# Performance work log

Hardware: AMD Instinct MI355X
Metric: run time of the kernel (lower is better)

The kernel has to match this reference:

```python
import jax, jax.numpy as jnp
import numpy as np

B, N, C = 16, 1024, 256
SIZE = (512, 640)          # (H, W) image size
STRIDE = 8
H0, W0 = SIZE[0] // STRIDE, SIZE[1] // STRIDE   # 64, 80
P_TOK = H0 * W0                                  # 5120 base tokens
NHEAD, NLVL, NPTS = 8, 4, 4
HD = C // NHEAD
NUM_CLASSES = 7


def setup_inputs() -> dict:
    key = jax.random.key(0)
    ks = jax.random.split(key, 16)
    g = lambda k, shape, s=0.02: jax.random.normal(k, shape, jnp.float32) * s
    return {
        "q_t": jax.random.normal(ks[0], (B, N, C), jnp.float32),
        "h_t": jax.random.normal(ks[1], (B, P_TOK, C), jnp.float32),
        "p_head_t": jax.random.uniform(ks[2], (B, N, 2), jnp.float32)
                    * jnp.array([SIZE[1], SIZE[0]], jnp.float32),  # (x,y) in image coords
        "W_off": g(ks[3], (C, NHEAD * NLVL * NPTS * 2)),
        "b_off": g(ks[4], (NHEAD * NLVL * NPTS * 2,)),
        "W_attn": g(ks[5], (C, NHEAD * NLVL * NPTS)),
        "b_attn": g(ks[6], (NHEAD * NLVL * NPTS,)),
        "W_v": g(ks[7], (C, C)), "b_v": g(ks[8], (C,)),
        "W_o": g(ks[9], (C, C)), "b_o": g(ks[10], (C,)),
        "W_p1": g(ks[11], (2 * C, C)), "b_p1": g(ks[12], (C,)),
        "W_p2": g(ks[13], (C, NUM_CLASSES)), "b_p2": g(ks[14], (NUM_CLASSES,)),
    }


def _bilinear_sample(value_l, loc):
    """value_l: (B,Hl,Wl,nh,hd); loc: (B,N,nh,NPTS,2) in [0,1] normalized (x,y).
    grid_sample semantics: align_corners=False, padding_mode='zeros'.
    Returns (B,nh,N,NPTS,hd)."""
    Bb, Hl, Wl = value_l.shape[0], value_l.shape[1], value_l.shape[2]
    x = loc[..., 0] * Wl - 0.5
    y = loc[..., 1] * Hl - 0.5
    x0 = jnp.floor(x); y0 = jnp.floor(y)
    wx = x - x0; wy = y - y0
    x0i = x0.astype(jnp.int32); y0i = y0.astype(jnp.int32)
    flat = value_l.reshape(Bb, Hl * Wl, NHEAD, HD).transpose(0, 2, 1, 3)  # (B,nh,S,hd)

    def corner(xi, yi):
        valid = ((xi >= 0) & (xi < Wl) & (yi >= 0) & (yi < Hl)).astype(value_l.dtype)
        idx = (jnp.clip(yi, 0, Hl - 1) * Wl + jnp.clip(xi, 0, Wl - 1)).transpose(0, 2, 1, 3)  # (B,nh,N,P)
        g = jnp.take_along_axis(flat, idx.reshape(Bb, NHEAD, -1)[..., None], axis=2)
        g = g.reshape(Bb, NHEAD, idx.shape[2], idx.shape[3], HD)
        return g * valid.transpose(0, 2, 1, 3)[..., None]

    tw = lambda w: w.transpose(0, 2, 1, 3)[..., None]  # (B,nh,N,P,1)
    return (corner(x0i, y0i) * tw((1 - wx) * (1 - wy))
            + corner(x0i + 1, y0i) * tw(wx * (1 - wy))
            + corner(x0i, y0i + 1) * tw((1 - wx) * wy)
            + corner(x0i + 1, y0i + 1) * tw(wx * wy))


def reference(q_t, h_t, p_head_t, W_off, b_off, W_attn, b_attn,
              W_v, b_v, W_o, b_o, W_p1, b_p1, W_p2, b_p2):
    # normalize point predictions to [0,1] (x by W, y by H)
    p_norm = jnp.clip(p_head_t / jnp.array([SIZE[1], SIZE[0]], jnp.float32), 0.0, 1.0)

    # ---- get_deformable_inputs: 4-level pyramid by 2x2 average pooling ----
    cur = h_t.reshape(B, H0, W0, C)
    feats, shapes = [], []
    for l in range(NLVL):
        feats.append(cur)
        shapes.append((cur.shape[1], cur.shape[2]))
        if l < NLVL - 1:
            h, w = cur.shape[1], cur.shape[2]
            cur = cur.reshape(B, h // 2, 2, w // 2, 2, C).mean(axis=(2, 4))
    f_scales = jnp.concatenate([f.reshape(B, -1, C) for f in feats], axis=1)  # (B,S,C)

    # ---- DMSMHA_Block (multi-scale deformable attention) ----
    value = (f_scales @ W_v + b_v).reshape(B, -1, NHEAD, HD)
    offsets = (q_t @ W_off + b_off).reshape(B, N, NHEAD, NLVL, NPTS, 2)
    attn = jax.nn.softmax(
        (q_t @ W_attn + b_attn).reshape(B, N, NHEAD, NLVL * NPTS), axis=-1
    ).reshape(B, N, NHEAD, NLVL, NPTS)

    out = jnp.zeros((B, NHEAD, N, HD), jnp.float32)
    start = 0
    for l, (Hl, Wl) in enumerate(shapes):
        Sl = Hl * Wl
        vl = value[:, start:start + Sl].reshape(B, Hl, Wl, NHEAD, HD)
        start += Sl
        norm = jnp.array([Wl, Hl], jnp.float32)
        loc = p_norm[:, :, None, None, :] + offsets[:, :, :, l] / norm  # (B,N,nh,P,2)
        sampled = _bilinear_sample(vl, loc)                              # (B,nh,N,P,hd)
        w = attn[:, :, :, l].transpose(0, 2, 1, 3)                       # (B,nh,N,P)
        out = out + jnp.einsum('bhnp,bhnpd->bhnd', w, sampled)

    q_local = out.transpose(0, 2, 1, 3).reshape(B, N, C) @ W_o + b_o

    # ---- fuse + MLP head ----
    q_fused = jnp.concatenate([q_t, q_local], axis=-1)
    hid = jax.nn.relu(q_fused @ W_p1 + b_p1)
    logits = hid @ W_p2 + b_p2   # (B,N,num_classes)
    return logits
```

## Files before the change

### kernel.cpp

```cpp
#include <hip/hip_runtime.h>
#include <math.h>


namespace {

constexpr int kB = 16;
constexpr int kN = 1024;
constexpr int kC = 256;
constexpr int kNCLS = 7;
constexpr int kSTOT = 6800;

typedef __attribute__((ext_vector_type(8))) short short8;
typedef __attribute__((ext_vector_type(4))) float f32x4;

__device__ inline ushort f2bf(float f) {
  union { float f; unsigned u; } v; v.f = f;
  unsigned r = (v.u + 0x7fffu + ((v.u >> 16) & 1u)) >> 16;
  return (ushort)r;
}
__device__ inline float bf2f(ushort h) {
  union { unsigned u; float f; } v; v.u = ((unsigned)h) << 16;
  return v.f;
}

__device__ inline void gload16(const ushort* g, ushort* l) {
  __builtin_amdgcn_global_load_lds(
      (const __attribute__((address_space(1))) void*)g,
      (__attribute__((address_space(3))) void*)l, 16, 0, 0);
}

__global__ void cast_f2b_kernel(const float* __restrict__ in, ushort* __restrict__ out, int n4) {
  int i = blockIdx.x * 256 + threadIdx.x;
  if (i >= n4) return;
  float4 v = ((const float4*)in)[i];
  ((ushort4*)out)[i] = make_ushort4(f2bf(v.x), f2bf(v.y), f2bf(v.z), f2bf(v.w));
}

__global__ void cast_pool_kernel(const float* __restrict__ h, ushort* __restrict__ fsc) {
  int i = blockIdx.x * 256 + threadIdx.x;
  if (i >= kB * 32 * 40 * 64) return;
  int cq = i & 63;
  int t = i >> 6;
  int x = t % 40; t /= 40;
  int y = t % 32; int b = t / 32;
  const float* base = h + (((size_t)b * 5120 + (2 * y) * 80 + 2 * x) << 8) + (cq << 2);
  float4 v00 = *(const float4*)(base);
  float4 v01 = *(const float4*)(base + 256);
  float4 v10 = *(const float4*)(base + 80 * 256);
  float4 v11 = *(const float4*)(base + 80 * 256 + 256);
  ushort* f0 = fsc + (((size_t)b * kSTOT + (2 * y) * 80 + 2 * x) << 8) + (cq << 2);
  *(ushort4*)(f0) = make_ushort4(f2bf(v00.x), f2bf(v00.y), f2bf(v00.z), f2bf(v00.w));
  *(ushort4*)(f0 + 256) = make_ushort4(f2bf(v01.x), f2bf(v01.y), f2bf(v01.z), f2bf(v01.w));
  *(ushort4*)(f0 + 80 * 256) = make_ushort4(f2bf(v10.x), f2bf(v10.y), f2bf(v10.z), f2bf(v10.w));
  *(ushort4*)(f0 + 80 * 256 + 256) =
      make_ushort4(f2bf(v11.x), f2bf(v11.y), f2bf(v11.z), f2bf(v11.w));
  float4 pv = make_float4(0.25f * (v00.x + v01.x + v10.x + v11.x),
                          0.25f * (v00.y + v01.y + v10.y + v11.y),
                          0.25f * (v00.z + v01.z + v10.z + v11.z),
                          0.25f * (v00.w + v01.w + v10.w + v11.w));
  ushort* f1 = fsc + (((size_t)b * kSTOT + 5120 + y * 40 + x) << 8) + (cq << 2);
  *(ushort4*)(f1) = make_ushort4(f2bf(pv.x), f2bf(pv.y), f2bf(pv.z), f2bf(pv.w));
}

__global__ void pool_b2b_kernel(const ushort* __restrict__ fin, ushort* __restrict__ fout,
                                int oh, int ow, int so_in, int so_out) {
  int idx = blockIdx.x * 256 + threadIdx.x;
  if (idx >= kB * oh * ow * kC) return;
  int c = idx & 255; int t = idx >> 8;
  int x = t % ow; t /= ow; int y = t % oh; int b = t / oh;
  int iw = ow * 2;
  const ushort* p = fin + (((size_t)b * kSTOT + so_in + y * 2 * iw + x * 2) << 8) + c;
  float s = 0.25f * (bf2f(p[0]) + bf2f(p[256]) + bf2f(p[iw * 256]) + bf2f(p[iw * 256 + 256]));
  fout[(((size_t)b * kSTOT + so_out + y * ow + x) << 8) + c] = f2bf(s);
}

__global__ void wtrans_all_kernel(const float* __restrict__ s0, const float* __restrict__ s1,
                                  const float* __restrict__ s2, const float* __restrict__ s3,
                                  const float* __restrict__ s4,
                                  ushort* __restrict__ d0, ushort* __restrict__ d1,
                                  ushort* __restrict__ d2, ushort* __restrict__ d3,
                                  ushort* __restrict__ d4) {
  __shared__ float t[32][33];
  const float* W; ushort* Wt; int K, N;
  switch (blockIdx.z) {
    case 0: W = s0; Wt = d0; K = 256; N = 256; break;
    case 1: W = s1; Wt = d1; K = 256; N = 256; break;
    case 2: W = s2; Wt = d2; K = 256; N = 128; break;
    case 3: W = s3; Wt = d3; K = 256; N = 256; break;
    default: W = s4; Wt = d4; K = 512; N = 256; break;
  }
  int nx = blockIdx.x << 5, ky = blockIdx.y << 5;
  if (nx >= N || ky >= K) return;
  int lx = threadIdx.x & 31, ly = threadIdx.x >> 5;
#pragma unroll
  for (int i = 0; i < 32; i += 8)
    t[ly + i][lx] = W[(size_t)(ky + ly + i) * N + nx + lx];
  __syncthreads();
#pragma unroll
  for (int i = 0; i < 32; i += 8)
    Wt[(size_t)(nx + ly + i) * K + ky + lx] = f2bf(t[lx][ly + i]);
}

template <int KTOT, bool SPLITK, int OMODE, bool RELU>
__global__ __launch_bounds__(256) void gemm_bf16_kernel(
    const ushort* __restrict__ A, const ushort* __restrict__ A2,
    const ushort* __restrict__ Wt, const float* __restrict__ bias,
    const float* __restrict__ bias2, void* __restrict__ Cout,
    void* __restrict__ Cout2, int ldc) {
  __shared__ ushort Asm[2][128 * 32];
  __shared__ ushort Bsm[2][128 * 32];
  const int tid = threadIdx.x;
  const int w = tid >> 6, l = tid & 63;
  const int bm = blockIdx.y << 7, bn = blockIdx.x << 7;
  const int wm = w >> 1, wn = w & 1;

  const int c0 = w * 2, c1 = w * 2 + 1;
  const int G0 = c0 * 64 + l, G1 = c1 * 64 + l;
  const int r0 = G0 >> 2, g0 = G0 & 3;
  const int r1 = G1 >> 2, g1 = G1 & 3;
  const int sz0 = (g0 ^ ((r0 >> 1) & 3)) << 3;
  const int sz1 = (g1 ^ ((r1 >> 1) & 3)) << 3;
  const int ak = SPLITK ? 256 : KTOT;
  const ushort* sA0 = A + (size_t)(bm + r0) * ak + sz0;
  const ushort* sA1 = A + (size_t)(bm + r1) * ak + sz1;
  const ushort* sA0b = SPLITK ? A2 + (size_t)(bm + r0) * 256 + sz0 : nullptr;
  const ushort* sA1b = SPLITK ? A2 + (size_t)(bm + r1) * 256 + sz1 : nullptr;
  const ushort* sB0 = Wt + (size_t)(bn + r0) * KTOT + sz0;
  const ushort* sB1 = Wt + (size_t)(bn + r1) * KTOT + sz1;

  const int e = l >> 4, rl = l & 15;
  int aoff[4], boff[4];
#pragma unroll
  for (int i = 0; i < 4; ++i) {
    int r = wm * 64 + i * 16 + rl;
    aoff[i] = r * 32 + ((e ^ ((r >> 1) & 3)) << 3);
    int rb = wn * 64 + i * 16 + rl;
    boff[i] = rb * 32 + ((e ^ ((rb >> 1) & 3)) << 3);
  }

  f32x4 acc[4][4];
#pragma unroll
  for (int i = 0; i < 4; ++i)
#pragma unroll
    for (int j = 0; j < 4; ++j) acc[i][j] = (f32x4){0.f, 0.f, 0.f, 0.f};

  auto stage = [&](int buf, int k0) {
    const ushort *a0, *a1;
    if (SPLITK && k0 >= 256) {
      a0 = sA0b + (k0 - 256);
      a1 = sA1b + (k0 - 256);
    } else {
      a0 = sA0 + k0;
      a1 = sA1 + k0;
    }
    gload16(a0, &Asm[buf][c0 * 512]);
    gload16(a1, &Asm[buf][c1 * 512]);
    gload16(sB0 + k0, &Bsm[buf][c0 * 512]);
    gload16(sB1 + k0, &Bsm[buf][c1 * 512]);
  };

  constexpr int nt = KTOT / 32;
  stage(0, 0);
  __syncthreads();
  for (int t = 0; t < nt; ++t) {
    const int cur = t & 1;
    if (t + 1 < nt) stage(cur ^ 1, (t + 1) * 32);
    short8 af[4], bfr[4];
#pragma unroll
    for (int i = 0; i < 4; ++i) af[i] = *(const short8*)&Asm[cur][aoff[i]];
#pragma unroll
    for (int j = 0; j < 4; ++j) bfr[j] = *(const short8*)&Bsm[cur][boff[j]];
#pragma unroll
    for (int i = 0; i < 4; ++i)
#pragma unroll
      for (int j = 0; j < 4; ++j)
        acc[i][j] = __builtin_amdgcn_mfma_f32_16x16x32_bf16(bfr[j], af[i], acc[i][j], 0, 0, 0);
    __syncthreads();
  }

#pragma unroll
  for (int j = 0; j < 4; ++j) {
    int ch = bn + wn * 64 + j * 16 + e * 4;
    float4 b4;
    if (OMODE == 2)
      b4 = (ch < 256) ? *(const float4*)(bias + ch) : *(const float4*)(bias2 + ch - 256);
    else
      b4 = *(const float4*)(bias + ch);
    float bv[4] = {b4.x, b4.y, b4.z, b4.w};
#pragma unroll
    for (int i = 0; i < 4; ++i) {
      int sp = bm + wm * 64 + i * 16 + rl;
      float v[4];
#pragma unroll
      for (int r = 0; r < 4; ++r) {
        v[r] = acc[i][j][r] + bv[r];
        if (RELU) v[r] = fmaxf(v[r], 0.f);
      }
      if (OMODE == 0) {
        *(float4*)&((float*)Cout)[(size_t)sp * ldc + ch] = make_float4(v[0], v[1], v[2], v[3]);
      } else if (OMODE == 1) {
        *(ushort4*)&((ushort*)Cout)[(size_t)sp * ldc + ch] =
            make_ushort4(f2bf(v[0]), f2bf(v[1]), f2bf(v[2]), f2bf(v[3]));
      } else {
        if (ch < 256)
          *(float4*)&((float*)Cout)[(size_t)sp * 256 + ch] = make_float4(v[0], v[1], v[2], v[3]);
        else
          *(float4*)&((float*)Cout2)[(size_t)sp * 128 + (ch - 256)] =
              make_float4(v[0], v[1], v[2], v[3]);
      }
    }
  }
}

__global__ void deform_kernel(
    const ushort* __restrict__ value, const float* __restrict__ off,
    const float* __restrict__ attnl, const float* __restrict__ p_head,
    ushort* __restrict__ samp) {
  int blk = (int)blockIdx.x;
  int sw = (blk & 7) * 256 + (blk >> 3);
  int wvi = (sw << 2) + (threadIdx.x >> 6);
  int l = threadIdx.x & 63;
  int nq = l >> 5;
  int lh = l & 31;
  int h = lh >> 2;
  int pt = wvi * 2 + nq;
  int b = pt >> 10;
  size_t bn = (size_t)pt;

  float ph = (lh < 2) ? p_head[bn * 2 + lh] : 0.f;
  float px = __shfl(ph, (nq << 5) + 0, 64) * (1.0f / 640.0f);
  float py = __shfl(ph, (nq << 5) + 1, 64) * (1.0f / 512.0f);
  px = fminf(fmaxf(px, 0.f), 1.f);
  py = fminf(fmaxf(py, 0.f), 1.f);

  const float4* offp = (const float4*)(off + (bn << 8));
  float4 ofv0 = offp[2 * lh];
  float4 ofv1 = offp[2 * lh + 1];
  float4 atv = ((const float4*)(attnl + (bn << 7)))[lh];

  float m = fmaxf(fmaxf(atv.x, atv.y), fmaxf(atv.z, atv.w));
  m = fmaxf(m, __shfl_xor(m, 1, 64));
  m = fmaxf(m, __shfl_xor(m, 2, 64));
  float e0 = expf(atv.x - m), e1 = expf(atv.y - m);
  float e2 = expf(atv.z - m), e3 = expf(atv.w - m);
  float s = e0 + e1 + e2 + e3;
  s += __shfl_xor(s, 1, 64);
  s += __shfl_xor(s, 2, 64);
  float inv = 1.f / s;
  atv = make_float4(e0 * inv, e1 * inv, e2 * inv, e3 * inv);

  float acc[8];
#pragma unroll
  for (int i = 0; i < 8; ++i) acc[i] = 0.f;
  const ushort* vbb = value + (((size_t)b * kSTOT) << 8) + (lh << 3);

#pragma unroll 1
  for (int lv = 0; lv < 4; ++lv) {
    const int Wl = 80 >> lv, Hl = 64 >> lv;
    const int offL = (lv == 0) ? 0 : (lv == 1) ? 5120 : (lv == 2) ? 6400 : 6720;
    const ushort* vb = vbb + (((size_t)offL) << 8);
    const int src = (nq << 5) + (h << 2) + lv;
    const float fx = px * (float)Wl - 0.5f;
    const float fy = py * (float)Hl - 0.5f;
#pragma unroll
    for (int pp = 0; pp < 4; ++pp) {
      float sx, sy;
      if ((pp >> 1) == 0) {
        sx = (pp & 1) ? ofv0.z : ofv0.x;
        sy = (pp & 1) ? ofv0.w : ofv0.y;
      } else {
        sx = (pp & 1) ? ofv1.z : ofv1.x;
        sy = (pp & 1) ? ofv1.w : ofv1.y;
      }
      float ox = __shfl(sx, src, 64);
      float oy = __shfl(sy, src, 64);
      float sa = pp == 0 ? atv.x : pp == 1 ? atv.y : pp == 2 ? atv.z : atv.w;
      float aw = __shfl(sa, src, 64);

      float xx = fx + ox;
      float yy = fy + oy;
      float x0f = floorf(xx), y0f = floorf(yy);
      float wx = xx - x0f, wy = yy - y0f;
      int x0 = (int)x0f, y0 = (int)y0f;
      float w00 = (1.f - wx) * (1.f - wy) * aw;
      float w01 = wx * (1.f - wy) * aw;
      float w10 = (1.f - wx) * wy * aw;
      float w11 = wx * wy * aw;
      auto corner = [&](int xi, int yi, float wgt) {
        bool valid = (xi >= 0) && (xi < Wl) && (yi >= 0) && (yi < Hl);
        int xc = xi < 0 ? 0 : (xi > Wl - 1 ? Wl - 1 : xi);
        int yc = yi < 0 ? 0 : (yi > Hl - 1 ? Hl - 1 : yi);
        short8 d = *(const short8*)(vb + (((size_t)(yc * Wl + xc)) << 8));
        float wg = valid ? wgt : 0.f;
#pragma unroll
        for (int i = 0; i < 8; ++i) acc[i] = fmaf(wg, bf2f((ushort)d[i]), acc[i]);
      };
      corner(x0, y0, w00);
      corner(x0 + 1, y0, w01);
      corner(x0, y0 + 1, w10);
      corner(x0 + 1, y0 + 1, w11);
    }
  }
  ushort o[8];
#pragma unroll
  for (int i = 0; i < 8; ++i) o[i] = f2bf(acc[i]);
  *(short8*)(samp + (bn << 8) + (lh << 3)) =
      (short8){(short)o[0], (short)o[1], (short)o[2], (short)o[3],
               (short)o[4], (short)o[5], (short)o[6], (short)o[7]};
}

__global__ void head_kernel(const float* __restrict__ hid, const float* __restrict__ W2,
                            const float* __restrict__ b2, float* __restrict__ outp) {
  int gid = blockIdx.x * 256 + threadIdx.x;
  int wave = gid >> 6;
  int lane = threadIdx.x & 63;
  if (wave >= kB * kN) return;
  const float* hrow = hid + ((size_t)wave << 8);
  float acc[kNCLS];
#pragma unroll
  for (int j = 0; j < kNCLS; ++j) acc[j] = 0.f;
  for (int k = lane; k < kC; k += 64) {
    float hv = hrow[k];
    const float* wr = W2 + k * kNCLS;
#pragma unroll
    for (int j = 0; j < kNCLS; ++j) acc[j] = fmaf(hv, wr[j], acc[j]);
  }
#pragma unroll
  for (int m = 32; m > 0; m >>= 1) {
#pragma unroll
    for (int j = 0; j < kNCLS; ++j) acc[j] += __shfl_xor(acc[j], m);
  }
  float r = 0.f;
#pragma unroll
  for (int j = 0; j < kNCLS; ++j)
    if (lane == j) r = acc[j] + b2[j];
  if (lane < kNCLS) outp[(size_t)wave * kNCLS + lane] = r;
}

}

extern "C" void kernel_launch(void* const* d_in, const int* in_sizes, int n_in,
                              void* d_out, int out_size, void* d_ws, size_t ws_size,
                              hipStream_t stream) {
  const float* q_t    = (const float*)d_in[0];
  const float* h_t    = (const float*)d_in[1];
  const float* p_head = (const float*)d_in[2];
  const float* W_off  = (const float*)d_in[3];
  const float* b_off  = (const float*)d_in[4];
  const float* W_attn = (const float*)d_in[5];
  const float* b_attn = (const float*)d_in[6];
  const float* W_v    = (const float*)d_in[7];
  const float* b_v    = (const float*)d_in[8];
  const float* W_o    = (const float*)d_in[9];
  const float* b_o    = (const float*)d_in[10];
  const float* W_p1   = (const float*)d_in[11];
  const float* b_p1   = (const float*)d_in[12];
  const float* W_p2   = (const float*)d_in[13];
  const float* b_p2   = (const float*)d_in[14];
  float* out = (float*)d_out;
  char* wsb = (char*)d_ws;

  ushort* fsc   = (ushort*)(wsb + 0);
  ushort* value = (ushort*)(wsb + 55705600);
  ushort* q_bf  = (ushort*)(wsb + 111411200);
  float*  offb  = (float*)(wsb + 119799808);
  float*  attnl = (float*)(wsb + 136577024);
  ushort* samp  = (ushort*)(wsb + 144965632);
  ushort* qloc  = (ushort*)(wsb + 153354240);
  float*  hid   = (float*)(wsb + 161742848);
  ushort* wtp   = (ushort*)(wsb + 178520064);
  ushort* Wt_v  = wtp;
  ushort* Wt_oa = wtp + 65536;
  ushort* Wt_o  = wtp + 163840;
  ushort* Wt_p1 = wtp + 229376;

  cast_f2b_kernel<<<4096, 256, 0, stream>>>(q_t, q_bf, kB * kN * 64);
  cast_pool_kernel<<<5120, 256, 0, stream>>>(h_t, fsc);
  pool_b2b_kernel<<<5120, 256, 0, stream>>>(fsc, fsc, 16, 20, 5120, 6400);
  pool_b2b_kernel<<<1280, 256, 0, stream>>>(fsc, fsc, 8, 10, 6400, 6720);

  wtrans_all_kernel<<<dim3(8, 16, 5), 256, 0, stream>>>(
      W_v, W_off, W_attn, W_o, W_p1,
      Wt_v, Wt_oa, Wt_oa + 65536, Wt_o, Wt_p1);

  gemm_bf16_kernel<256, false, 1, false><<<dim3(2, 850), 256, 0, stream>>>(
      fsc, nullptr, Wt_v, b_v, nullptr, value, nullptr, 256);

  gemm_bf16_kernel<256, false, 2, false><<<dim3(3, 128), 256, 0, stream>>>(
      q_bf, nullptr, Wt_oa, b_off, b_attn, offb, attnl, 256);

  deform_kernel<<<2048, 256, 0, stream>>>(value, offb, attnl, p_head, samp);

  gemm_bf16_kernel<256, false, 1, false><<<dim3(2, 128), 256, 0, stream>>>(
      samp, nullptr, Wt_o, b_o, nullptr, qloc, nullptr, 256);

  gemm_bf16_kernel<512, true, 0, true><<<dim3(2, 128), 256, 0, stream>>>(
      q_bf, qloc, Wt_p1, b_p1, nullptr, hid, nullptr, 256);

  head_kernel<<<4096, 256, 0, stream>>>(hid, W_p2, b_p2, out);
}
```

Baseline: 158.4 us.

## Add dedicated 256x128-tile double-buffered bf16 GEMM for value projection

Replaces the generic GEMM used for the value projection (108800x256 by 256x256) with a specialized kernel that uses a 256-row by 128-column block tile. It double-buffers LDS with XOR-swizzled layout and issues 8x4 MFMA 16x16x32 tiles per wave. The larger tile halves the number of blocks and raises arithmetic intensity per loaded byte. In exchange it uses more registers (128 accumulator floats per thread) and more LDS, which lowers occupancy.

```diff
diff --git a/kernel.cpp b/kernel.cpp
--- a/kernel.cpp
+++ b/kernel.cpp
@@ -212,6 +212,90 @@
   }
 }
 
+__global__ __launch_bounds__(256) void gemm256_kernel(
+    const ushort* __restrict__ A, const ushort* __restrict__ Wt,
+    const float* __restrict__ bias, ushort* __restrict__ Cout) {
+  __shared__ ushort Asm[2][256 * 32];
+  __shared__ ushort Bsm[2][128 * 32];
+  const int tid = threadIdx.x;
+  const int w = tid >> 6, l = tid & 63;
+  const int bm = blockIdx.y << 8, bn = blockIdx.x << 7;
+  const int wm = w >> 1, wn = w & 1;
+
+  const ushort* sA[4];
+  const ushort* sB[2];
+#pragma unroll
+  for (int k = 0; k < 4; ++k) {
+    int G = (w * 4 + k) * 64 + l, r = G >> 2, g = G & 3;
+    sA[k] = A + (size_t)(bm + r) * 256 + ((g ^ ((r >> 1) & 3)) << 3);
+  }
+#pragma unroll
+  for (int k = 0; k < 2; ++k) {
+    int G = (w * 2 + k) * 64 + l, r = G >> 2, g = G & 3;
+    sB[k] = Wt + (size_t)(bn + r) * 256 + ((g ^ ((r >> 1) & 3)) << 3);
+  }
+
+  const int e = l >> 4, rl = l & 15;
+  int aoff[8], boff[4];
+#pragma unroll
+  for (int i = 0; i < 8; ++i) {
+    int r = wm * 128 + i * 16 + rl;
+    aoff[i] = r * 32 + ((e ^ ((r >> 1) & 3)) << 3);
+  }
+#pragma unroll
+  for (int j = 0; j < 4; ++j) {
+    int rb = wn * 64 + j * 16 + rl;
+    boff[j] = rb * 32 + ((e ^ ((rb >> 1) & 3)) << 3);
+  }
+
+  f32x4 acc[8][4];
+#pragma unroll
+  for (int i = 0; i < 8; ++i)
+#pragma unroll
+    for (int j = 0; j < 4; ++j) acc[i][j] = (f32x4){0.f, 0.f, 0.f, 0.f};
+
+  auto stage = [&](int buf, int k0) {
+#pragma unroll
+    for (int k = 0; k < 4; ++k) gload16(sA[k] + k0, &Asm[buf][(w * 4 + k) * 512]);
+#pragma unroll
+    for (int k = 0; k < 2; ++k) gload16(sB[k] + k0, &Bsm[buf][(w * 2 + k) * 512]);
+  };
+
+  stage(0, 0);
+  __syncthreads();
+  for (int t = 0; t < 8; ++t) {
+    const int cur = t & 1;
+    if (t < 7) stage(cur ^ 1, (t + 1) * 32);
+    short8 af[8], bfr[4];
+#pragma unroll
+    for (int i = 0; i < 8; ++i) af[i] = *(const short8*)&Asm[cur][aoff[i]];
+#pragma unroll
+    for (int j = 0; j < 4; ++j) bfr[j] = *(const short8*)&Bsm[cur][boff[j]];
+#pragma unroll
+    for (int i = 0; i < 8; ++i)
+#pragma unroll
+      for (int j = 0; j < 4; ++j)
+        acc[i][j] = __builtin_amdgcn_mfma_f32_16x16x32_bf16(bfr[j], af[i], acc[i][j], 0, 0, 0);
+    __syncthreads();
+  }
+
+#pragma unroll
+  for (int j = 0; j < 4; ++j) {
+    int ch = bn + wn * 64 + j * 16 + e * 4;
+    float4 b4 = *(const float4*)(bias + ch);
+    float bv[4] = {b4.x, b4.y, b4.z, b4.w};
+#pragma unroll
+    for (int i = 0; i < 8; ++i) {
+      int sp = bm + wm * 128 + i * 16 + rl;
+      float v[4];
+#pragma unroll
+      for (int r = 0; r < 4; ++r) v[r] = acc[i][j][r] + bv[r];
+      *(ushort4*)&Cout[(size_t)sp * 256 + ch] =
+          make_ushort4(f2bf(v[0]), f2bf(v[1]), f2bf(v[2]), f2bf(v[3]));
+    }
+  }
+}
+
 __global__ void deform_kernel(
     const ushort* __restrict__ value, const float* __restrict__ off,
     const float* __restrict__ attnl, const float* __restrict__ p_head,
@@ -383,8 +467,7 @@
       W_v, W_off, W_attn, W_o, W_p1,
       Wt_v, Wt_oa, Wt_oa + 65536, Wt_o, Wt_p1);
 
-  gemm_bf16_kernel<256, false, 1, false><<<dim3(2, 850), 256, 0, stream>>>(
-      fsc, nullptr, Wt_v, b_v, nullptr, value, nullptr, 256);
+  gemm256_kernel<<<dim3(2, 425), 256, 0, stream>>>(fsc, Wt_v, b_v, value);
 
   gemm_bf16_kernel<256, false, 2, false><<<dim3(3, 128), 256, 0, stream>>>(
       q_bf, nullptr, Wt_oa, b_off, b_attn, offb, attnl, 256);
```

Measured after the change: 182.4 us. 1.15x slower.
